# Kernel optimization log

Hardware: AMD Instinct MI355X
Metric: run time of the kernel (lower is better)

Reference implementation:

```python
import jax, jax.numpy as jnp
import numpy as np

KSIZE = 3
STRIDE = 1
PADDING = 1
DILATION = 1
C_IN = 16
C_OUT = 16


def setup_inputs() -> dict:
    key = jax.random.key(0)
    k1, k2, k3 = jax.random.split(key, 3)
    inputs = jax.random.normal(k1, (2, C_IN, 24, 24, 24, 24), dtype=jnp.float32)
    weight = jax.random.normal(k2, (C_OUT, C_IN * KSIZE ** 4), dtype=jnp.float32)
    bias = jax.random.normal(k3, (1, C_OUT, 1, 1, 1, 1), dtype=jnp.float32)
    return {"inputs": inputs, "weight": weight, "bias": bias}


def reference(inputs, weight, bias):
    # weight stored flattened: [C_out, C_in * k^4] -> [C_out, C_in, k, k, k, k]
    w = weight.reshape(C_OUT, C_IN, KSIZE, KSIZE, KSIZE, KSIZE)
    # General 4-spatial-dim convolution via XLA's ND conv.
    dn = jax.lax.ConvDimensionNumbers(
        lhs_spec=(0, 1, 2, 3, 4, 5),   # N, C, U, V, H, W
        rhs_spec=(0, 1, 2, 3, 4, 5),   # O, I, kU, kV, kH, kW
        out_spec=(0, 1, 2, 3, 4, 5),
    )
    out = jax.lax.conv_general_dilated(
        inputs, w,
        window_strides=(STRIDE,) * 4,
        padding=((PADDING, PADDING),) * 4,
        rhs_dilation=(DILATION,) * 4,
        dimension_numbers=dn,
    )
    return out + bias
```

## Files before the change

### kernel.cpp

```cpp
#include <hip/hip_runtime.h>

#define S 24
#define PLANE 576
#define CISTRIDE 331776
#define SLAB_B 21632
#define A_BYTES 46080
#define WS_SLABS A_BYTES

typedef __attribute__((ext_vector_type(8))) short bf16x8;
typedef __attribute__((ext_vector_type(4))) float f32x4;

__device__ __forceinline__ ushort f2bf(float f) {
    unsigned int u = __builtin_bit_cast(unsigned int, f);
    unsigned int r = u + 0x7fffu + ((u >> 16) & 1u);
    return (ushort)(r >> 16);
}

__device__ __forceinline__ int swz(int row, int col, int half) {
    return (((row * 26 + col) * 32) + half * 16) ^ ((row & 3) << 4);
}

__global__ void __launch_bounds__(256)
pack_in(const float* __restrict__ in, const float* __restrict__ wgt, char* __restrict__ ws) {
    __shared__ unsigned lds_t[16][288];

    const int b = blockIdx.x;
    const int nb = b / PLANE, uv = b % PLANE;
    const float* src = in + (size_t)nb * 16 * CISTRIDE + (size_t)uv * PLANE;
    char* dst = ws + WS_SLABS + (size_t)b * SLAB_B;
    const int t = threadIdx.x;

    #pragma unroll
    for (int i = 0; i < 9; ++i) {
        int flat = i * 256 + t;
        int ci = flat / 144, q4 = flat % 144;
        float4 f = *(const float4*)(src + (size_t)ci * CISTRIDE + 4 * q4);
        uint2 pk;
        pk.x = (unsigned)f2bf(f.x) | ((unsigned)f2bf(f.y) << 16);
        pk.y = (unsigned)f2bf(f.z) | ((unsigned)f2bf(f.w) << 16);
        *(uint2*)&lds_t[ci][2 * q4] = pk;
    }
    __syncthreads();

    #pragma unroll
    for (int i = 0; i < 6; ++i) {
        int c = i * 256 + t;
        if (c < 1352) {
            int k = c >> 2;
            int row = k / 13;
            int pos2 = c ^ (row & 3);
            int pos = pos2 >> 1, h = pos2 & 1;
            int col = pos - row * 26;
            uint4 o = make_uint4(0, 0, 0, 0);
            if (row >= 1 && row <= 24 && col >= 1 && col <= 24) {
                int q = (row - 1) * 24 + (col - 1);
                int q2 = q >> 1, odd = q & 1;
                #pragma unroll
                for (int kk = 0; kk < 4; ++kk) {
                    unsigned a = lds_t[8 * h + 2 * kk][q2];
                    unsigned bb = lds_t[8 * h + 2 * kk + 1][q2];
                    unsigned val = odd ? ((a >> 16) | (bb & 0xffff0000u))
                                       : ((a & 0xffffu) | (bb << 16));
                    ((unsigned*)&o)[kk] = val;
                }
            }
            *(uint4*)(dst + (size_t)c * 16) = o;
        }
    }

    if (b == 0) {
        for (int i = t; i < 2880; i += 256) {
            int step = i >> 6;
            int tap = step / 5, s = step % 5;
            int lane = i & 63;
            int co = lane & 15, gA = lane >> 4;
            int o = 2 * s + (gA >> 1);
            int cib = (gA & 1) * 8;
            ushort vals[8];
            #pragma unroll
            for (int j = 0; j < 8; ++j)
                vals[j] = (o <= 8) ? f2bf(wgt[co * 1296 + (cib + j) * 81 + tap * 9 + o]) : (ushort)0;
            uint4 pk;
            pk.x = vals[0] | ((unsigned)vals[1] << 16);
            pk.y = vals[2] | ((unsigned)vals[3] << 16);
            pk.z = vals[4] | ((unsigned)vals[5] << 16);
            pk.w = vals[6] | ((unsigned)vals[7] << 16);
            *(uint4*)(ws + (size_t)i * 16) = pk;
        }
    }
}

__global__ void __launch_bounds__(256, 3)
conv4d_main(const char* __restrict__ ws, const float* __restrict__ bias,
            float* __restrict__ out) {
    __shared__ __align__(16) char lds[2 * SLAB_B];

    const int t = threadIdx.x, lane = t & 63, wvid = t >> 6;
    const int braw = blockIdx.x;
    const int b = (braw & 7) * 72 + (braw >> 3);
    const int nb = b / 288, rem = b % 288;
    const int u = rem / 12, v0 = (rem % 12) * 2;

    const int n16 = lane & 15, g = lane >> 4;
    const int dh = n16 >> 2, dw = n16 & 3;
    const int half = g & 1, osel = g >> 1;

    int laneoff[5];
    #pragma unroll
    for (int s = 0; s < 5; ++s) {
        int o = 2 * s + osel; if (o > 8) o = 8;
        int kh = o / 3, kw = o % 3;
        laneoff[s] = swz(dh + kh, dw + kw, half);
    }
    const int wv_off = (wvid >> 1) * 9984 + (wvid & 1) * 384;

    f32x4 acc0[9], acc1[9];
    #pragma unroll
    for (int i = 0; i < 9; ++i) { acc0[i] = (f32x4){0,0,0,0}; acc1[i] = (f32x4){0,0,0,0}; }

    unsigned mask = 0;
    #pragma unroll
    for (int i = 0; i < 12; ++i) {
        int uu = u + (i >> 2) - 1, vv = v0 + (i & 3) - 1;
        if (uu >= 0 && uu < S && vv >= 0 && vv < S) mask |= 1u << i;
    }

    const char* slabs = ws + WS_SLABS;
    #define SLAB_PTR(i_) (slabs + ((size_t)nb * PLANE + (u + ((i_) >> 2) - 1) * S + (v0 + ((i_) & 3) - 1)) * SLAB_B)

    #define STAGE(bufsel_, src_) do {                                              \
        const char* _s = (src_);                                                   \
        _Pragma("unroll")                                                          \
        for (int r2 = 0; r2 < 6; ++r2) {                                           \
            int chunk = r2 * 256 + t;                                              \
            if (r2 < 5 || t < 72)                                                  \
                __builtin_amdgcn_global_load_lds(                                  \
                    (const __attribute__((address_space(1))) unsigned int*)(_s + (size_t)chunk * 16), \
                    (__attribute__((address_space(3))) unsigned int*)(lds + (bufsel_) * SLAB_B + chunk * 16), \
                    16, 0, 0);                                                     \
        }                                                                          \
    } while (0)

    const bf16x8 zfr = {0,0,0,0,0,0,0,0};

    int cur = __ffs(mask) - 1;
    int bufsel = 0;
    STAGE(0, SLAB_PTR(cur));
    __syncthreads();

    while (1) {
        unsigned remm = mask >> (cur + 1);
        int nxt = remm ? (cur + 1 + __ffs(remm) - 1) : -1;
        if (nxt >= 0) STAGE(bufsel ^ 1, SLAB_PTR(nxt));

        const int ku = cur >> 2, dv = (cur & 3) - 1;
        const bool v0ok = dv <= 1, v1ok = dv >= 0;
        const char* ap0 = ws + (size_t)(ku * 3 + dv + 1) * 5120 + (size_t)lane * 16;
        const char* ap1 = ws + (size_t)(ku * 3 + dv) * 5120 + (size_t)lane * 16;
        bf16x8 afr0[5], afr1[5];
        #pragma unroll
        for (int s = 0; s < 5; ++s) {
            afr0[s] = v0ok ? *(const bf16x8*)(ap0 + s * 1024) : zfr;
            afr1[s] = v1ok ? *(const bf16x8*)(ap1 + s * 1024) : zfr;
        }

        const char* bp = lds + bufsel * SLAB_B + wv_off;
        #pragma unroll
        for (int ti = 0; ti < 9; ++ti) {
            const int timm = (ti / 3) * 3328 + (ti % 3) * 128;
            #pragma unroll
            for (int s = 0; s < 5; ++s) {
                bf16x8 bfr = *(const bf16x8*)(bp + timm + laneoff[s]);
                acc0[ti] = __builtin_amdgcn_mfma_f32_16x16x32_bf16(afr0[s], bfr, acc0[ti], 0, 0, 0);
                acc1[ti] = __builtin_amdgcn_mfma_f32_16x16x32_bf16(afr1[s], bfr, acc1[ti], 0, 0, 0);
            }
        }
        __syncthreads();
        if (nxt < 0) break;
        cur = nxt; bufsel ^= 1;
    }

    float bv[4];
    #pragma unroll
    for (int r = 0; r < 4; ++r) bv[r] = bias[g * 4 + r];
    float* outp0 = out + (size_t)nb * 16 * CISTRIDE + (size_t)(u * S + v0) * PLANE;
    float* outp1 = outp0 + PLANE;
    #pragma unroll
    for (int ti = 0; ti < 9; ++ti) {
        int h0 = ((ti / 3) + (wvid >> 1) * 3) * 4;
        int w0 = ((ti % 3) + (wvid & 1) * 3) * 4;
        int pos = (h0 + dh) * S + (w0 + dw);
        #pragma unroll
        for (int r = 0; r < 4; ++r) {
            outp0[(size_t)(g * 4 + r) * CISTRIDE + pos] = acc0[ti][r] + bv[r];
            outp1[(size_t)(g * 4 + r) * CISTRIDE + pos] = acc1[ti][r] + bv[r];
        }
    }
}

extern "C" void kernel_launch(void* const* d_in, const int* in_sizes, int n_in,
                              void* d_out, int out_size, void* d_ws, size_t ws_size,
                              hipStream_t stream) {
    const float* in   = (const float*)d_in[0];
    const float* wgt  = (const float*)d_in[1];
    const float* bias = (const float*)d_in[2];
    float* out        = (float*)d_out;
    char* ws          = (char*)d_ws;

    pack_in<<<dim3(2 * PLANE), dim3(256), 0, stream>>>(in, wgt, ws);
    conv4d_main<<<dim3(576), dim3(256), 0, stream>>>(ws, bias, out);
}
```

Before: 85.03 us.

## Split each output block into H-halves with 2x8 tiles and three waves

The main conv kernel now splits each (u, v-pair) output block into two halves along H, giving twice as many blocks of 192 threads. Each block stages only the half-slab it needs into LDS, and each wave computes six 2x8 spatial tiles instead of nine 4x4 tiles. The aims are more parallelism across the GPU, a smaller LDS footprint so more blocks fit per CU, and wider contiguous output rows for the stores. In exchange the overlapping halo rows are loaded from global memory twice, and the swizzled LDS offsets have to be recomputed for the new tile shape.

```diff
diff --git a/kernel.cpp b/kernel.cpp
--- a/kernel.cpp
+++ b/kernel.cpp
@@ -4,6 +4,8 @@
 #define PLANE 576
 #define CISTRIDE 331776
 #define SLAB_B 21632
+#define HSLAB_B 11648
+#define HOFF 9984
 #define A_BYTES 46080
 #define WS_SLABS A_BYTES
 
@@ -90,33 +92,37 @@
     }
 }
 
-__global__ void __launch_bounds__(256, 3)
+__global__ void __launch_bounds__(192, 4)
 conv4d_main(const char* __restrict__ ws, const float* __restrict__ bias,
             float* __restrict__ out) {
-    __shared__ __align__(16) char lds[2 * SLAB_B];
+    __shared__ __align__(16) char lds[2 * HSLAB_B];
 
     const int t = threadIdx.x, lane = t & 63, wvid = t >> 6;
     const int braw = blockIdx.x;
-    const int b = (braw & 7) * 72 + (braw >> 3);
-    const int nb = b / 288, rem = b % 288;
-    const int u = rem / 12, v0 = (rem % 12) * 2;
+    const int b = (braw & 7) * 144 + (braw >> 3);
+    const int nb = b / 576, rem = b % 576;
+    const int u = rem / 24, rem2 = rem % 24;
+    const int v0 = (rem2 >> 1) * 2, hh = rem2 & 1;
 
     const int n16 = lane & 15, g = lane >> 4;
-    const int dh = n16 >> 2, dw = n16 & 3;
+    const int dh = n16 >> 3, dw = n16 & 7;
     const int half = g & 1, osel = g >> 1;
 
-    int laneoff[5];
-    #pragma unroll
-    for (int s = 0; s < 5; ++s) {
-        int o = 2 * s + osel; if (o > 8) o = 8;
-        int kh = o / 3, kw = o % 3;
-        laneoff[s] = swz(dh + kh, dw + kw, half);
-    }
-    const int wv_off = (wvid >> 1) * 9984 + (wvid & 1) * 384;
-
-    f32x4 acc0[9], acc1[9];
-    #pragma unroll
-    for (int i = 0; i < 9; ++i) { acc0[i] = (f32x4){0,0,0,0}; acc1[i] = (f32x4){0,0,0,0}; }
+    int laneoff[2][5];
+    #pragma unroll
+    for (int trp = 0; trp < 2; ++trp)
+        #pragma unroll
+        for (int s = 0; s < 5; ++s) {
+            int o = 2 * s + osel; if (o > 8) o = 8;
+            int kh = o / 3, kw = o % 3;
+            int r_off = dh + kh, c_off = dw + kw;
+            int lin = (r_off * 26 + c_off) * 32 + half * 16;
+            laneoff[trp][s] = lin ^ ((((trp << 1) + r_off) & 3) << 4);
+        }
+
+    f32x4 acc0[6], acc1[6];
+    #pragma unroll
+    for (int i = 0; i < 6; ++i) { acc0[i] = (f32x4){0,0,0,0}; acc1[i] = (f32x4){0,0,0,0}; }
 
     unsigned mask = 0;
     #pragma unroll
@@ -126,17 +132,18 @@
     }
 
     const char* slabs = ws + WS_SLABS;
-    #define SLAB_PTR(i_) (slabs + ((size_t)nb * PLANE + (u + ((i_) >> 2) - 1) * S + (v0 + ((i_) & 3) - 1)) * SLAB_B)
+    const int srcoff = hh * HOFF;
+    #define SLAB_PTR(i_) (slabs + ((size_t)nb * PLANE + (u + ((i_) >> 2) - 1) * S + (v0 + ((i_) & 3) - 1)) * SLAB_B + srcoff)
 
     #define STAGE(bufsel_, src_) do {                                              \
         const char* _s = (src_);                                                   \
         _Pragma("unroll")                                                          \
-        for (int r2 = 0; r2 < 6; ++r2) {                                           \
-            int chunk = r2 * 256 + t;                                              \
-            if (r2 < 5 || t < 72)                                                  \
+        for (int r2 = 0; r2 < 4; ++r2) {                                           \
+            int chunk = r2 * 192 + t;                                              \
+            if (r2 < 3 || t < 152)                                                 \
                 __builtin_amdgcn_global_load_lds(                                  \
                     (const __attribute__((address_space(1))) unsigned int*)(_s + (size_t)chunk * 16), \
-                    (__attribute__((address_space(3))) unsigned int*)(lds + (bufsel_) * SLAB_B + chunk * 16), \
+                    (__attribute__((address_space(3))) unsigned int*)(lds + (bufsel_) * HSLAB_B + chunk * 16), \
                     16, 0, 0);                                                     \
         }                                                                          \
     } while (0)
@@ -164,15 +171,19 @@
             afr1[s] = v1ok ? *(const bf16x8*)(ap1 + s * 1024) : zfr;
         }
 
-        const char* bp = lds + bufsel * SLAB_B + wv_off;
-        #pragma unroll
-        for (int ti = 0; ti < 9; ++ti) {
-            const int timm = (ti / 3) * 3328 + (ti % 3) * 128;
+        const char* bp = lds + bufsel * HSLAB_B + wvid * 3328;
+        #pragma unroll
+        for (int tr = 0; tr < 2; ++tr) {
             #pragma unroll
-            for (int s = 0; s < 5; ++s) {
-                bf16x8 bfr = *(const bf16x8*)(bp + timm + laneoff[s]);
-                acc0[ti] = __builtin_amdgcn_mfma_f32_16x16x32_bf16(afr0[s], bfr, acc0[ti], 0, 0, 0);
-                acc1[ti] = __builtin_amdgcn_mfma_f32_16x16x32_bf16(afr1[s], bfr, acc1[ti], 0, 0, 0);
+            for (int tc = 0; tc < 3; ++tc) {
+                const int ti = tr * 3 + tc;
+                const char* bpt = bp + tr * 1664 + tc * 256;
+                #pragma unroll
+                for (int s = 0; s < 5; ++s) {
+                    bf16x8 bfr = *(const bf16x8*)(bpt + laneoff[tr][s]);
+                    acc0[ti] = __builtin_amdgcn_mfma_f32_16x16x32_bf16(afr0[s], bfr, acc0[ti], 0, 0, 0);
+                    acc1[ti] = __builtin_amdgcn_mfma_f32_16x16x32_bf16(afr1[s], bfr, acc1[ti], 0, 0, 0);
+                }
             }
         }
         __syncthreads();
@@ -186,14 +197,18 @@
     float* outp0 = out + (size_t)nb * 16 * CISTRIDE + (size_t)(u * S + v0) * PLANE;
     float* outp1 = outp0 + PLANE;
     #pragma unroll
-    for (int ti = 0; ti < 9; ++ti) {
-        int h0 = ((ti / 3) + (wvid >> 1) * 3) * 4;
-        int w0 = ((ti % 3) + (wvid & 1) * 3) * 4;
-        int pos = (h0 + dh) * S + (w0 + dw);
-        #pragma unroll
-        for (int r = 0; r < 4; ++r) {
-            outp0[(size_t)(g * 4 + r) * CISTRIDE + pos] = acc0[ti][r] + bv[r];
-            outp1[(size_t)(g * 4 + r) * CISTRIDE + pos] = acc1[ti][r] + bv[r];
+    for (int tr = 0; tr < 2; ++tr) {
+        #pragma unroll
+        for (int tc = 0; tc < 3; ++tc) {
+            const int ti = tr * 3 + tc;
+            int row = hh * 12 + wvid * 4 + tr * 2 + dh;
+            int col = tc * 8 + dw;
+            int pos = row * S + col;
+            #pragma unroll
+            for (int r = 0; r < 4; ++r) {
+                outp0[(size_t)(g * 4 + r) * CISTRIDE + pos] = acc0[ti][r] + bv[r];
+                outp1[(size_t)(g * 4 + r) * CISTRIDE + pos] = acc1[ti][r] + bv[r];
+            }
         }
     }
 }
@@ -208,5 +223,5 @@
     char* ws          = (char*)d_ws;
 
     pack_in<<<dim3(2 * PLANE), dim3(256), 0, stream>>>(in, wgt, ws);
-    conv4d_main<<<dim3(576), dim3(256), 0, stream>>>(ws, bias, out);
-}
+    conv4d_main<<<dim3(1152), dim3(192), 0, stream>>>(ws, bias, out);
+}
```

After: 77.43 us. 8.9% less time.
